# Performance work log

Hardware: AMD Instinct MI355X
Metric: run time of the kernel (lower is better)

The kernel has to match this reference:

```python
import jax, jax.numpy as jnp
import numpy as np
from jax import lax

B, C, L, H = 32, 256, 1280, 5
D = L // H  # head dim = 256
EPS = 1e-5


def setup_inputs() -> dict:
    key = jax.random.key(0)
    ks = jax.random.split(key, 16)
    s = 0.02
    inp = {
        "x": jax.random.normal(ks[0], (B, C, L), jnp.float32),
        # rank encoder Linear(L, L)
        "re_w": jax.random.normal(ks[1], (L, L), jnp.float32) * s,
        "re_b": jnp.zeros((L,), jnp.float32),
        # layer norms
        "ln1_g": jnp.ones((L,), jnp.float32), "ln1_b": jnp.zeros((L,), jnp.float32),
        "ln2_g": jnp.ones((L,), jnp.float32), "ln2_b": jnp.zeros((L,), jnp.float32),
        # attention projections (stored [in, out]; y @ W + b)
        "wq": jax.random.normal(ks[2], (L, L), jnp.float32) * s, "bq": jnp.zeros((L,), jnp.float32),
        "wk": jax.random.normal(ks[3], (L, L), jnp.float32) * s, "bk": jnp.zeros((L,), jnp.float32),
        "wv": jax.random.normal(ks[4], (L, L), jnp.float32) * s, "bv": jnp.zeros((L,), jnp.float32),
        "wo": jax.random.normal(ks[5], (L, L), jnp.float32) * s, "bo": jnp.zeros((L,), jnp.float32),
        # FFN (ffn_size == hidden_size == L in this module)
        "ffn_w1": jax.random.normal(ks[6], (L, L), jnp.float32) * s, "ffn_b1": jnp.zeros((L,), jnp.float32),
        "ffn_w2": jax.random.normal(ks[7], (L, L), jnp.float32) * s, "ffn_b2": jnp.zeros((L,), jnp.float32),
        # Conv1d(C, C, k=3, stride=1, pad=1, bias=False) + BatchNorm1d (eval) + ReLU
        "conv_w": jax.random.normal(ks[8], (C, C, 3), jnp.float32) * (2.0 / (C * 3)) ** 0.5,
        "bn_g": jnp.ones((C,), jnp.float32), "bn_b": jnp.zeros((C,), jnp.float32),
        "bn_m": jnp.zeros((C,), jnp.float32), "bn_v": jnp.ones((C,), jnp.float32),
    }
    return inp


def _layernorm(t, g, b):
    m = jnp.mean(t, axis=-1, keepdims=True)
    v = jnp.var(t, axis=-1, keepdims=True)
    return (t - m) * lax.rsqrt(v + EPS) * g + b


def reference(x, re_w, re_b, ln1_g, ln1_b, ln2_g, ln2_b,
              wq, bq, wk, bk, wv, bv, wo, bo,
              ffn_w1, ffn_b1, ffn_w2, ffn_b2,
              conv_w, bn_g, bn_b, bn_m, bn_v):
    b_, c_, l_ = x.shape
    # _getrank_: rank from double argsort (descending), mapped to (L - rank)/L
    rank_i = jnp.argsort(jnp.argsort(-x, axis=-1), axis=-1)
    rank = (l_ - rank_i).astype(x.dtype) / l_
    node = x + rank @ re_w + re_b                      # [B, C, L]

    # EncoderLayer: pre-LN MHSA (attn_bias is None in this call path)
    y = _layernorm(node, ln1_g, ln1_b)
    scale = D ** -0.5
    q = (y @ wq + bq).reshape(b_, c_, H, D).transpose(0, 2, 1, 3) * scale  # [B,H,C,D]
    k = (y @ wk + bk).reshape(b_, c_, H, D).transpose(0, 2, 1, 3)
    v = (y @ wv + bv).reshape(b_, c_, H, D).transpose(0, 2, 1, 3)
    attn = jax.nn.softmax(jnp.einsum('bhqd,bhkd->bhqk', q, k), axis=-1)   # [B,H,C,C]
    o = jnp.einsum('bhqk,bhkd->bhqd', attn, v)
    o = o.transpose(0, 2, 1, 3).reshape(b_, c_, l_) @ wo + bo
    h = node + o  # dropout is identity in eval

    # FFN sublayer
    y2 = _layernorm(h, ln2_g, ln2_b)
    f = jax.nn.gelu(y2 @ ffn_w1 + ffn_b1, approximate=False) @ ffn_w2 + ffn_b2
    h = h + f                                           # [B, C, L]

    # ConvBNRelu: Conv1d(k=3, s=1, p=1, no bias) -> BN (eval stats) -> ReLU
    conv = lax.conv_general_dilated(h, conv_w, window_strides=(1,),
                                    padding=[(1, 1)],
                                    dimension_numbers=('NCH', 'OIH', 'NCH'))
    bn = (conv - bn_m[None, :, None]) * lax.rsqrt(bn_v[None, :, None] + EPS)
    bn = bn * bn_g[None, :, None] + bn_b[None, :, None]
    return jax.nn.relu(bn)
```

## Files before the change

kernel.cpp:

```cpp
#include <hip/hip_runtime.h>
#include <hip/hip_bf16.h>
#include <stdint.h>

#define L_   1280
#define B_   32
#define C_   256
#define H_   5
#define D_   256
#define BC_  8192
#define EPSV 1e-5f

typedef __attribute__((ext_vector_type(8))) short bf16x8;
typedef __attribute__((ext_vector_type(4))) float f32x4;
typedef __hip_bfloat16 bf16;

__device__ __forceinline__ bf16 f2bf(float v) { return __float2bfloat16(v); }

#define GLDS16(gptr, lptr)                                                        \
    __builtin_amdgcn_global_load_lds(                                             \
        (const __attribute__((address_space(1))) void*)(gptr),                    \
        (__attribute__((address_space(3))) void*)(lptr), 16, 0, 0)

struct WtArgs { const float* src[7]; bf16* dst[7]; };

__global__ __launch_bounds__(256) void transpose7(WtArgs a) {
    const int mat = blockIdx.z;
    const float* src = a.src[mat];
    bf16* dst = a.dst[mat];
    __shared__ float tile[32][33];
    const int bx = blockIdx.x * 32;
    const int by = blockIdx.y * 32;
    const int tx = threadIdx.x, ty = threadIdx.y;
    #pragma unroll
    for (int r = ty; r < 32; r += 8)
        tile[r][tx] = src[(size_t)(by + r) * L_ + bx + tx];
    __syncthreads();
    #pragma unroll
    for (int r = ty; r < 32; r += 8)
        dst[(size_t)(bx + r) * L_ + by + tx] = f2bf(tile[tx][r]);
}

__global__ __launch_bounds__(256) void prep_conv(const float* cw, const float* g, const float* b,
                                                 const float* m, const float* v,
                                                 bf16* WT, float* sc, float* bi) {
    const int i = blockIdx.x * 256 + threadIdx.x;
    if (i < 3 * 256 * 256) {
        const int co = i / 768;
        const int r = i - co * 768;
        const int t = r >> 8, ci = r & 255;
        WT[i] = f2bf(cw[(co * 256 + ci) * 3 + t]);
    }
    if (i < 256) {
        const float s = g[i] * rsqrtf(v[i] + EPSV);
        sc[i] = s;
        bi[i] = b[i] - m[i] * s;
    }
}

__global__ __launch_bounds__(256) void rank_kernel(const float* __restrict__ x, bf16* __restrict__ R) {
    __shared__ float vals[L_];
    __shared__ float sv[L_];
    __shared__ int hist[256];
    __shared__ int pfx[256];
    __shared__ int cur[256];
    const int row = blockIdx.x, tid = threadIdx.x;
    const float* src = x + (size_t)row * L_;
    for (int i = tid; i < L_; i += 256) vals[i] = src[i];
    hist[tid] = 0;
    __syncthreads();
    float myv[5]; int myb[5];
    #pragma unroll
    for (int ii = 0; ii < 5; ii++) {
        const float v = vals[tid + ii * 256];
        int bk = (int)((4.0f - v) * 32.0f);
        bk = bk < 0 ? 0 : (bk > 255 ? 255 : bk);
        myv[ii] = v; myb[ii] = bk;
        atomicAdd(&hist[bk], 1);
    }
    __syncthreads();
    pfx[tid] = hist[tid];
    __syncthreads();
    for (int off = 1; off < 256; off <<= 1) {
        int t = (tid >= off) ? pfx[tid - off] : 0;
        __syncthreads();
        pfx[tid] += t;
        __syncthreads();
    }
    cur[tid] = pfx[tid] - hist[tid];
    __syncthreads();
    #pragma unroll
    for (int ii = 0; ii < 5; ii++) {
        const int pos = atomicAdd(&cur[myb[ii]], 1);
        sv[pos] = myv[ii];
    }
    __syncthreads();
    #pragma unroll
    for (int ii = 0; ii < 5; ii++) {
        const int bk = myb[ii]; const float v = myv[ii];
        const int s = pfx[bk] - hist[bk], e = pfx[bk];
        int cg = s;
        for (int p = s; p < e; p++) cg += (sv[p] > v) ? 1 : 0;
        R[(size_t)row * L_ + tid + ii * 256] = f2bf((float)(L_ - cg) * (1.0f / L_));
    }
}

__global__ __launch_bounds__(256) void ln_kernel(const float* __restrict__ in,
                                                 const float* __restrict__ g,
                                                 const float* __restrict__ b,
                                                 bf16* __restrict__ out) {
    const int row = blockIdx.x, tid = threadIdx.x;
    const float* src = in + (size_t)row * L_;
    float4 va = ((const float4*)src)[tid];
    float s = va.x + va.y + va.z + va.w;
    float ss = va.x * va.x + va.y * va.y + va.z * va.z + va.w * va.w;
    float4 vb = {0, 0, 0, 0};
    if (tid < 64) {
        vb = ((const float4*)src)[256 + tid];
        s += vb.x + vb.y + vb.z + vb.w;
        ss += vb.x * vb.x + vb.y * vb.y + vb.z * vb.z + vb.w * vb.w;
    }
    #pragma unroll
    for (int off = 32; off > 0; off >>= 1) {
        s += __shfl_down(s, off, 64);
        ss += __shfl_down(ss, off, 64);
    }
    __shared__ float rs[4], rss[4];
    __shared__ float mean_s, rstd_s;
    if ((tid & 63) == 0) { rs[tid >> 6] = s; rss[tid >> 6] = ss; }
    __syncthreads();
    if (tid == 0) {
        const float S = rs[0] + rs[1] + rs[2] + rs[3];
        const float SS = rss[0] + rss[1] + rss[2] + rss[3];
        const float m = S * (1.0f / L_);
        const float var = SS * (1.0f / L_) - m * m;
        mean_s = m; rstd_s = rsqrtf(var + EPSV);
    }
    __syncthreads();
    const float m = mean_s, r = rstd_s;
    {
        const int c = tid * 4;
        bf16 t4[4];
        t4[0] = f2bf((va.x - m) * r * g[c + 0] + b[c + 0]);
        t4[1] = f2bf((va.y - m) * r * g[c + 1] + b[c + 1]);
        t4[2] = f2bf((va.z - m) * r * g[c + 2] + b[c + 2]);
        t4[3] = f2bf((va.w - m) * r * g[c + 3] + b[c + 3]);
        *(uint2*)(out + (size_t)row * L_ + c) = *(uint2*)t4;
    }
    if (tid < 64) {
        const int c = 1024 + tid * 4;
        bf16 t4[4];
        t4[0] = f2bf((vb.x - m) * r * g[c + 0] + b[c + 0]);
        t4[1] = f2bf((vb.y - m) * r * g[c + 1] + b[c + 1]);
        t4[2] = f2bf((vb.z - m) * r * g[c + 2] + b[c + 2]);
        t4[3] = f2bf((vb.w - m) * r * g[c + 3] + b[c + 3]);
        *(uint2*)(out + (size_t)row * L_ + c) = *(uint2*)t4;
    }
}

__global__ __launch_bounds__(256) void softmax_kernel(const bf16* __restrict__ S, bf16* __restrict__ P) {
    const int row = blockIdx.x * 4 + (threadIdx.x >> 6);
    const int l = threadIdx.x & 63;
    const bf16* src = S + (size_t)row * 256 + l * 4;
    uint2 raw = *(const uint2*)src;
    bf16 s4[4]; *(uint2*)s4 = raw;
    float v0 = __bfloat162float(s4[0]), v1 = __bfloat162float(s4[1]);
    float v2 = __bfloat162float(s4[2]), v3 = __bfloat162float(s4[3]);
    float mx = fmaxf(fmaxf(v0, v1), fmaxf(v2, v3));
    #pragma unroll
    for (int off = 1; off < 64; off <<= 1) mx = fmaxf(mx, __shfl_xor(mx, off, 64));
    const float e0 = expf(v0 - mx), e1 = expf(v1 - mx), e2 = expf(v2 - mx), e3 = expf(v3 - mx);
    float sm = e0 + e1 + e2 + e3;
    #pragma unroll
    for (int off = 1; off < 64; off <<= 1) sm += __shfl_xor(sm, off, 64);
    const float inv = 1.0f / sm;
    bf16 t4[4] = { f2bf(e0 * inv), f2bf(e1 * inv), f2bf(e2 * inv), f2bf(e3 * inv) };
    *(uint2*)(P + (size_t)row * 256 + l * 4) = *(uint2*)t4;
}

__global__ __launch_bounds__(256) void zero_pads(bf16* h2T) {
    const int i = blockIdx.x * 256 + threadIdx.x;
    const int b = i >> 9;
    const int which = (i >> 8) & 1;
    const int ci = i & 255;
    const long row = which ? 1281 : 0;
    h2T[(long)b * (1282 * 256) + row * 256 + ci] = f2bf(0.0f);
}

struct GemmP {
    const bf16* A;  long lda, sA1, sA2;
    const bf16* Bt; long ldb, sB1, sB2;
    int zmod;
    int K;
    float* outF; bf16* outB; bf16* outB2; bf16* outB3; long ldc, sC1, sC2;
    const float* bias; const float* bias2; const float* bias3;
    const float* res; long ldres, sR1, sR2;
    const float* rowscale; const float* rowbias;
    float scale;
};

constexpr int E_F32_BIAS_RES = 0;
constexpr int E_F32 = 4;
constexpr int E_BF16 = 5;
constexpr int E_GELU = 6;
constexpr int E_FFN2T = 7;
constexpr int E_CONVBNR = 8;
constexpr int E_QKV = 9;

template <int EPI>
__global__ __launch_bounds__(256) void gemm_bt(GemmP p) {
    const int nwg  = gridDim.x * gridDim.y * gridDim.z;
    const int orig = (blockIdx.z * gridDim.y + blockIdx.y) * gridDim.x + blockIdx.x;
    const int qq = nwg >> 3, rr = nwg & 7;
    const int xcd = orig & 7, pos = orig >> 3;
    const int wgid = (xcd < rr ? xcd * (qq + 1) : rr * (qq + 1) + (xcd - rr) * qq) + pos;
    const int bx = wgid % gridDim.x;
    const int t1 = wgid / gridDim.x;
    const int by = t1 % gridDim.y;
    const int bz = t1 / gridDim.y;

    const int zq = bz / p.zmod, zr = bz % p.zmod;
    const bf16* A  = p.A  + (long)zq * p.sA1 + (long)zr * p.sA2;
    const bf16* Bt = p.Bt + (long)zq * p.sB1 + (long)zr * p.sB2;
    const int row0 = by * 128, col0 = bx * 128;

    __shared__ __align__(16) bf16 ldsA[2][128 * 32];
    __shared__ __align__(16) bf16 ldsB[2][128 * 32];

    const int tid = threadIdx.x;
    const int l = tid & 63, w = tid >> 6;
    const int wr = w >> 1, wc = w & 1;

    f32x4 acc[4][4];
    #pragma unroll
    for (int m = 0; m < 4; m++)
        #pragma unroll
        for (int n = 0; n < 4; n++)
            acc[m][n] = (f32x4){0.f, 0.f, 0.f, 0.f};

    const bf16* gA = A  + (long)(row0 + w * 16 + (l >> 2)) * p.lda + (l & 3) * 8;
    const bf16* gB = Bt + (long)(col0 + w * 16 + (l >> 2)) * p.ldb + (l & 3) * 8;
    const long aStep = 64 * p.lda, bStep = 64 * p.ldb;

    auto STAGE = [&](int buf) {
        GLDS16(gA,         &ldsA[buf][w * 512]);
        GLDS16(gA + aStep, &ldsA[buf][2048 + w * 512]);
        GLDS16(gB,         &ldsB[buf][w * 512]);
        GLDS16(gB + bStep, &ldsB[buf][2048 + w * 512]);
        gA += 32; gB += 32;
    };
    auto COMPUTE = [&](int buf) {
        bf16x8 aF[4], bF[4];
        #pragma unroll
        for (int m = 0; m < 4; m++)
            aF[m] = *(const bf16x8*)(&ldsA[buf][(wr * 64 + m * 16 + (l & 15)) * 32 + (l >> 4) * 8]);
        #pragma unroll
        for (int n = 0; n < 4; n++)
            bF[n] = *(const bf16x8*)(&ldsB[buf][(wc * 64 + n * 16 + (l & 15)) * 32 + (l >> 4) * 8]);
        #pragma unroll
        for (int m = 0; m < 4; m++)
            #pragma unroll
            for (int n = 0; n < 4; n++)
                acc[m][n] = __builtin_amdgcn_mfma_f32_16x16x32_bf16(aF[m], bF[n], acc[m][n], 0, 0, 0);
    };

    const int nt = p.K >> 5;
    STAGE(0);
    int cur = 0;
    for (int t = 0; t < nt - 1; ++t) {
        STAGE(cur ^ 1);
        asm volatile("s_waitcnt vmcnt(4)" ::: "memory");
        __builtin_amdgcn_sched_barrier(0);
        __builtin_amdgcn_s_barrier();
        COMPUTE(cur);
        __builtin_amdgcn_sched_barrier(0);
        __builtin_amdgcn_s_barrier();
        cur ^= 1;
    }
    asm volatile("s_waitcnt vmcnt(0)" ::: "memory");
    __builtin_amdgcn_sched_barrier(0);
    __builtin_amdgcn_s_barrier();
    COMPUTE(cur);

    const long cz = (long)zq * p.sC1 + (long)zr * p.sC2;
    const long rz = (long)zq * p.sR1 + (long)zr * p.sR2;
    #pragma unroll
    for (int m = 0; m < 4; m++) {
        #pragma unroll
        for (int n = 0; n < 4; n++) {
            const int gcol = col0 + wc * 64 + n * 16 + (l & 15);
            #pragma unroll
            for (int j = 0; j < 4; j++) {
                const int grow = row0 + wr * 64 + m * 16 + (l >> 4) * 4 + j;
                const float v = acc[m][n][j];
                if constexpr (EPI == E_F32_BIAS_RES) {
                    p.outF[cz + (long)grow * p.ldc + gcol] =
                        v + p.bias[gcol] + p.res[rz + (long)grow * p.ldres + gcol];
                } else if constexpr (EPI == E_F32) {
                    p.outF[cz + (long)grow * p.ldc + gcol] = v;
                } else if constexpr (EPI == E_BF16) {
                    p.outB[cz + (long)grow * p.ldc + gcol] = f2bf(v);
                } else if constexpr (EPI == E_GELU) {
                    const float t = v + p.bias[gcol];
                    p.outB[cz + (long)grow * p.ldc + gcol] =
                        f2bf(0.5f * t * (1.0f + erff(t * 0.70710678f)));
                } else if constexpr (EPI == E_FFN2T) {
                    const float t = v + p.bias[gcol] + p.res[rz + (long)grow * p.ldres + gcol];
                    const int b_ = grow >> 8, ci = grow & 255;
                    p.outB[(long)b_ * (1282 * 256) + (long)(gcol + 1) * 256 + ci] = f2bf(t);
                } else if constexpr (EPI == E_CONVBNR) {
                    const float t = v * p.rowscale[grow] + p.rowbias[grow];
                    p.outF[cz + (long)grow * p.ldc + gcol] = fmaxf(t, 0.0f);
                } else if constexpr (EPI == E_QKV) {
                    if (gcol < 1280) {
                        p.outB[(long)grow * L_ + gcol] = f2bf((v + p.bias[gcol]) * p.scale);
                    } else if (gcol < 2560) {
                        const int c2 = gcol - 1280;
                        p.outB2[(long)grow * L_ + c2] = f2bf(v + p.bias2[c2]);
                    } else {
                        const int c3 = gcol - 2560;
                        const int b_ = grow >> 8, c_ = grow & 255;
                        const int h_ = c3 >> 8, d_ = c3 & 255;
                        p.outB3[(((long)(b_ * H_ + h_) * 256 + d_) << 8) + c_] =
                            f2bf(v + p.bias3[c3]);
                    }
                }
            }
        }
    }
}

extern "C" void kernel_launch(void* const* d_in, const int* in_sizes, int n_in,
                              void* d_out, int out_size, void* d_ws, size_t ws_size,
                              hipStream_t stream) {
    const float* x    = (const float*)d_in[0];
    const float* re_w = (const float*)d_in[1];
    const float* re_b = (const float*)d_in[2];
    const float* ln1g = (const float*)d_in[3];
    const float* ln1b = (const float*)d_in[4];
    const float* ln2g = (const float*)d_in[5];
    const float* ln2b = (const float*)d_in[6];
    const float* wq   = (const float*)d_in[7];
    const float* bq   = (const float*)d_in[8];
    const float* wk   = (const float*)d_in[9];
    const float* bk   = (const float*)d_in[10];
    const float* wv   = (const float*)d_in[11];
    const float* bv   = (const float*)d_in[12];
    const float* wo   = (const float*)d_in[13];
    const float* bo   = (const float*)d_in[14];
    const float* fw1  = (const float*)d_in[15];
    const float* fb1  = (const float*)d_in[16];
    const float* fw2  = (const float*)d_in[17];
    const float* fb2  = (const float*)d_in[18];
    const float* convw = (const float*)d_in[19];
    const float* bng  = (const float*)d_in[20];
    const float* bnb  = (const float*)d_in[21];
    const float* bnm  = (const float*)d_in[22];
    const float* bnv  = (const float*)d_in[23];
    float* out = (float*)d_out;

    char* ws = (char*)d_ws;
    const size_t SZ_WT     = (size_t)L_ * L_ * 2;
    const size_t SZ_ACT_BF = (size_t)BC_ * L_ * 2;
    const size_t SZ_ACT_F  = (size_t)BC_ * L_ * 4;
    const size_t SZ_H2T    = (size_t)B_ * 1282 * 256 * 2;
    const size_t SZ_S      = (size_t)160 * 256 * 256 * 4;

    size_t off = 0;
    bf16* Wt[7];
    for (int i = 0; i < 7; i++) { Wt[i] = (bf16*)(ws + off); off += SZ_WT; }
    bf16* WconvT   = (bf16*)(ws + off); off += 393216;
    float* bnscale = (float*)(ws + off); off += 1024;
    float* bnbias  = (float*)(ws + off); off += 1024;
    bf16* RP  = (bf16*)(ws + off); off += SZ_ACT_BF;
    bf16* Yb  = (bf16*)(ws + off); off += SZ_ACT_BF;
    bf16* Qb  = (bf16*)(ws + off); off += SZ_ACT_BF;
    bf16* Kb  = (bf16*)(ws + off); off += SZ_H2T;
    float* Sb = (float*)(ws + off); off += SZ_S;
    float* node = (float*)(ws + off); off += SZ_ACT_F;
    bf16* Sbf = (bf16*)Sb;
    bf16* VT  = Sbf + (size_t)160 * 65536;
    (void)in_sizes; (void)n_in; (void)out_size;

    if (ws_size < off) return;

    WtArgs wa;
    wa.src[0] = re_w; wa.src[1] = wq; wa.src[2] = wk; wa.src[3] = wv;
    wa.src[4] = wo;  wa.src[5] = fw1; wa.src[6] = fw2;
    for (int i = 0; i < 7; i++) wa.dst[i] = Wt[i];
    transpose7<<<dim3(40, 40, 7), dim3(32, 8), 0, stream>>>(wa);
    prep_conv<<<dim3(768), 256, 0, stream>>>(convw, bng, bnb, bnm, bnv, WconvT, bnscale, bnbias);

    rank_kernel<<<dim3(BC_), 256, 0, stream>>>(x, RP);

    const dim3 gBig(L_ / 128, BC_ / 128, 1);
    const dim3 gQKV(3840 / 128, BC_ / 128, 1);
    const dim3 gAttn(2, 2, 160);
    const dim3 blk(256);

    {
        GemmP p{}; p.zmod = 1; p.K = L_;
        p.A = RP; p.lda = L_; p.Bt = Wt[0]; p.ldb = L_;
        p.outF = node; p.ldc = L_; p.bias = re_b; p.res = x; p.ldres = L_;
        gemm_bt<E_F32_BIAS_RES><<<gBig, blk, 0, stream>>>(p);
    }
    ln_kernel<<<dim3(BC_), blk, 0, stream>>>(node, ln1g, ln1b, Yb);
    {
        GemmP p{}; p.zmod = 1; p.K = L_;
        p.A = Yb; p.lda = L_; p.Bt = Wt[1]; p.ldb = L_;
        p.outB = Qb; p.outB2 = Kb; p.outB3 = VT;
        p.bias = bq; p.bias2 = bk; p.bias3 = bv; p.scale = 0.0625f;
        gemm_bt<E_QKV><<<gQKV, blk, 0, stream>>>(p);
    }
    {
        GemmP p{}; p.zmod = H_; p.K = 256;
        p.A = Qb;  p.lda = L_; p.sA1 = (long)C_ * L_; p.sA2 = 256;
        p.Bt = Kb; p.ldb = L_; p.sB1 = (long)C_ * L_; p.sB2 = 256;
        p.outB = Sbf; p.ldc = 256; p.sC1 = (long)H_ * 65536; p.sC2 = 65536;
        gemm_bt<E_BF16><<<gAttn, blk, 0, stream>>>(p);
    }
    softmax_kernel<<<dim3(160 * 256 / 4), blk, 0, stream>>>(Sbf, RP);
    {
        GemmP p{}; p.zmod = H_; p.K = 256;
        p.A = RP;  p.lda = 256; p.sA1 = (long)H_ * 65536; p.sA2 = 65536;
        p.Bt = VT; p.ldb = 256; p.sB1 = (long)H_ * 65536; p.sB2 = 65536;
        p.outB = Qb; p.ldc = L_; p.sC1 = (long)C_ * L_; p.sC2 = 256;
        gemm_bt<E_BF16><<<gAttn, blk, 0, stream>>>(p);
    }
    {
        GemmP p{}; p.zmod = 1; p.K = L_;
        p.A = Qb; p.lda = L_; p.Bt = Wt[4]; p.ldb = L_;
        p.outF = node; p.ldc = L_; p.bias = bo; p.res = node; p.ldres = L_;
        gemm_bt<E_F32_BIAS_RES><<<gBig, blk, 0, stream>>>(p);
    }
    ln_kernel<<<dim3(BC_), blk, 0, stream>>>(node, ln2g, ln2b, RP);
    {
        GemmP p{}; p.zmod = 1; p.K = L_;
        p.A = RP; p.lda = L_; p.Bt = Wt[5]; p.ldb = L_;
        p.outB = Yb; p.ldc = L_; p.bias = fb1;
        gemm_bt<E_GELU><<<gBig, blk, 0, stream>>>(p);
    }
    zero_pads<<<dim3(64), blk, 0, stream>>>(Kb);
    {
        GemmP p{}; p.zmod = 1; p.K = L_;
        p.A = Yb; p.lda = L_; p.Bt = Wt[6]; p.ldb = L_;
        p.outB = Kb; p.bias = fb2; p.res = node; p.ldres = L_;
        gemm_bt<E_FFN2T><<<gBig, blk, 0, stream>>>(p);
    }
    {
        GemmP p{}; p.zmod = 1; p.K = 768;
        p.A = WconvT; p.lda = 768;
        p.Bt = Kb; p.ldb = 256; p.sB1 = 1282 * 256;
        p.outF = out; p.ldc = L_; p.sC1 = (long)C_ * L_;
        p.rowscale = bnscale; p.rowbias = bnbias;
        gemm_bt<E_CONVBNR><<<dim3(L_ / 128, 2, B_), blk, 0, stream>>>(p);
    }
}
```

Before: 554.2 us.

## Transpose V-tile through LDS for coalesced stores and remap workgroups per XCD

The QKV GEMM epilogue for the V section now stages the 128x128 tile in LDS with an XOR swizzle, then writes it transposed as 16-byte vector stores instead of strided scalar bf16 stores. The workgroup-to-XCD mapping is also changed so that each XCD gets contiguous row groups sharing a column when the grid divides evenly, which should improve L2 reuse. LDS is unified into one buffer so it can be reused for the transpose, at the cost of an extra barrier pair in that epilogue.

```diff
diff --git a/kernel.cpp b/kernel.cpp
--- a/kernel.cpp
+++ b/kernel.cpp
@@ -210,21 +210,30 @@
 __global__ __launch_bounds__(256) void gemm_bt(GemmP p) {
     const int nwg  = gridDim.x * gridDim.y * gridDim.z;
     const int orig = (blockIdx.z * gridDim.y + blockIdx.y) * gridDim.x + blockIdx.x;
-    const int qq = nwg >> 3, rr = nwg & 7;
-    const int xcd = orig & 7, pos = orig >> 3;
-    const int wgid = (xcd < rr ? xcd * (qq + 1) : rr * (qq + 1) + (xcd - rr) * qq) + pos;
-    const int bx = wgid % gridDim.x;
-    const int t1 = wgid / gridDim.x;
-    const int by = t1 % gridDim.y;
-    const int bz = t1 / gridDim.y;
+    int bx, rowg;
+    if ((nwg & 7) == 0) {
+        const int chunk = nwg >> 3;
+        const int xcd = orig & 7, pos = orig >> 3;
+        const int rpc = chunk / gridDim.x;
+        if (rpc * gridDim.x == chunk) {
+            bx   = pos / rpc;
+            rowg = xcd * rpc + (pos - bx * rpc);
+        } else {
+            const int wgid = xcd * chunk + pos;
+            bx = wgid % gridDim.x; rowg = wgid / gridDim.x;
+        }
+    } else {
+        bx = blockIdx.x; rowg = blockIdx.z * gridDim.y + blockIdx.y;
+    }
+    const int by = rowg % gridDim.y;
+    const int bz = rowg / gridDim.y;
 
     const int zq = bz / p.zmod, zr = bz % p.zmod;
     const bf16* A  = p.A  + (long)zq * p.sA1 + (long)zr * p.sA2;
     const bf16* Bt = p.Bt + (long)zq * p.sB1 + (long)zr * p.sB2;
     const int row0 = by * 128, col0 = bx * 128;
 
-    __shared__ __align__(16) bf16 ldsA[2][128 * 32];
-    __shared__ __align__(16) bf16 ldsB[2][128 * 32];
+    __shared__ __align__(16) bf16 shm[16384];
 
     const int tid = threadIdx.x;
     const int l = tid & 63, w = tid >> 6;
@@ -242,20 +251,24 @@
     const long aStep = 64 * p.lda, bStep = 64 * p.ldb;
 
     auto STAGE = [&](int buf) {
-        GLDS16(gA,         &ldsA[buf][w * 512]);
-        GLDS16(gA + aStep, &ldsA[buf][2048 + w * 512]);
-        GLDS16(gB,         &ldsB[buf][w * 512]);
-        GLDS16(gB + bStep, &ldsB[buf][2048 + w * 512]);
+        bf16* lA = shm + buf * 4096;
+        bf16* lB = shm + 8192 + buf * 4096;
+        GLDS16(gA,         lA + w * 512);
+        GLDS16(gA + aStep, lA + 2048 + w * 512);
+        GLDS16(gB,         lB + w * 512);
+        GLDS16(gB + bStep, lB + 2048 + w * 512);
         gA += 32; gB += 32;
     };
     auto COMPUTE = [&](int buf) {
+        const bf16* lA = shm + buf * 4096;
+        const bf16* lB = shm + 8192 + buf * 4096;
         bf16x8 aF[4], bF[4];
         #pragma unroll
         for (int m = 0; m < 4; m++)
-            aF[m] = *(const bf16x8*)(&ldsA[buf][(wr * 64 + m * 16 + (l & 15)) * 32 + (l >> 4) * 8]);
+            aF[m] = *(const bf16x8*)(lA + (wr * 64 + m * 16 + (l & 15)) * 32 + (l >> 4) * 8);
         #pragma unroll
         for (int n = 0; n < 4; n++)
-            bF[n] = *(const bf16x8*)(&ldsB[buf][(wc * 64 + n * 16 + (l & 15)) * 32 + (l >> 4) * 8]);
+            bF[n] = *(const bf16x8*)(lB + (wc * 64 + n * 16 + (l & 15)) * 32 + (l >> 4) * 8);
         #pragma unroll
         for (int m = 0; m < 4; m++)
             #pragma unroll
@@ -280,6 +293,40 @@
     __builtin_amdgcn_sched_barrier(0);
     __builtin_amdgcn_s_barrier();
     COMPUTE(cur);
+
+    if constexpr (EPI == E_QKV) {
+        if (col0 >= 2560) {
+            const int v0  = col0 - 2560;
+            const int hh  = v0 >> 8;
+            const int dd0 = v0 & 255;
+            const int b_  = row0 >> 8;
+            const int c0b = row0 & 255;
+            __syncthreads();
+            #pragma unroll
+            for (int m = 0; m < 4; m++)
+                #pragma unroll
+                for (int n = 0; n < 4; n++) {
+                    const int cc = wc * 64 + n * 16 + (l & 15);
+                    const float bb = p.bias3[v0 + cc];
+                    #pragma unroll
+                    for (int j = 0; j < 4; j++) {
+                        const int r = wr * 64 + m * 16 + (l >> 4) * 4 + j;
+                        shm[cc * 128 + (r ^ ((cc & 7) << 3))] = f2bf(acc[m][n][j] + bb);
+                    }
+                }
+            __syncthreads();
+            const int d = tid >> 1, ch = (tid & 1) * 64;
+            bf16* dstRow = p.outB3 +
+                (((long)((b_ * H_ + hh) * 256 + dd0 + d)) << 8) + c0b;
+            #pragma unroll
+            for (int g = 0; g < 8; g++) {
+                const int rb = ch + g * 8;
+                *(bf16x8*)(dstRow + rb) =
+                    *(const bf16x8*)&shm[d * 128 + (rb ^ ((d & 7) << 3))];
+            }
+            return;
+        }
+    }
 
     const long cz = (long)zq * p.sC1 + (long)zr * p.sC2;
     const long rz = (long)zq * p.sR1 + (long)zr * p.sR2;
@@ -313,15 +360,9 @@
                 } else if constexpr (EPI == E_QKV) {
                     if (gcol < 1280) {
                         p.outB[(long)grow * L_ + gcol] = f2bf((v + p.bias[gcol]) * p.scale);
-                    } else if (gcol < 2560) {
+                    } else {
                         const int c2 = gcol - 1280;
                         p.outB2[(long)grow * L_ + c2] = f2bf(v + p.bias2[c2]);
-                    } else {
-                        const int c3 = gcol - 2560;
-                        const int b_ = grow >> 8, c_ = grow & 255;
-                        const int h_ = c3 >> 8, d_ = c3 & 255;
-                        p.outB3[(((long)(b_ * H_ + h_) * 256 + d_) << 8) + c_] =
-                            f2bf(v + p.bias3[c3]);
                     }
                 }
             }
```

Result: faster. 541.9 us (-2.2%).
